# Performance work log

Measured on AMD Instinct MI355X. Metric: run time of the kernel, lower is better.

The kernel has to match this reference:

```python
import jax, jax.numpy as jnp
import numpy as np

NUM_BEAMS = 2


def setup_inputs() -> dict:
    key = jax.random.key(0)
    ks = jax.random.split(key, 5)
    B, T, H, E, F = 128, 32, 768, 4, 3072
    x = jax.random.normal(ks[0], (B, T, H), dtype=jnp.float32)
    Wg = jax.random.normal(ks[1], (E, H), dtype=jnp.float32) * (1.0 / np.sqrt(H))
    W1 = jax.random.normal(ks[2], (E, H, F), dtype=jnp.float32) * (1.0 / np.sqrt(H))
    b1 = jnp.zeros((E, F), dtype=jnp.float32)
    W2 = jax.random.normal(ks[3], (E, F, H), dtype=jnp.float32) * (1.0 / np.sqrt(F))
    b2 = jnp.zeros((E, H), dtype=jnp.float32)
    return {"x": x, "Wg": Wg, "W1": W1, "b1": b1, "W2": W2, "b2": b2}


def reference(x, Wg, W1, b1, W2, b2):
    B, T, H = x.shape
    E = Wg.shape[0]
    nb = NUM_BEAMS
    # ---- forward_gate: mask is all-ones, so masked mean == mean over tokens ----
    x_avg = jnp.mean(x, axis=1)                          # [B, H]
    logits_gate = x_avg @ Wg.T                           # [B, E]
    prob_gate = jax.nn.softmax(logits_gate, axis=-1)     # [B, E]
    # ---- importance auxiliary loss (torch.std uses ddof=1) ----
    importance = jnp.sum(prob_gate, axis=0)              # [E]
    importance_loss = (jnp.std(importance, ddof=1) / jnp.mean(importance)) ** 2
    # ---- beam search, first layer: exp(log(p)) == p, top-k per row ----
    current_scores = jnp.exp(jnp.log(prob_gate))         # == prob_gate (kept for fidelity)
    topk_values, gate_idx = jax.lax.top_k(current_scores, nb)   # [B, nb]
    beam_scores = topk_values.reshape(nb * B)            # row-major flatten, matches .view
    expert_route = gate_idx.reshape(nb * B)[:, None]     # [B*nb, 1]
    beam_idx = jnp.arange(nb * B)
    current_expert_select = expert_route[:, -1]          # [B*nb]
    # ---- first layer: replicate x and scores along beam dim (interleaved) ----
    x_rep = jnp.repeat(x, nb, axis=0)                    # [B*nb, T, H]
    scores_rep = jnp.repeat(prob_gate, nb, axis=0)       # [B*nb, E]
    # input_x = x_rep[beam_idx] is identity here (beam_idx == arange)
    # ---- forward_expert_ffn: run ALL experts, mask+combine with gate prob ----
    h1 = jnp.einsum('bth,ehf->betf', x_rep, W1) + b1[None, :, None, :]
    h1 = jax.nn.gelu(h1, approximate=False)              # torch GELU is exact erf form
    cand = jnp.einsum('betf,efh->beth', h1, W2) + b2[None, :, None, :]  # [B*nb, E, T, H]
    weight = scores_rep * jax.nn.one_hot(current_expert_select, E, dtype=scores_rep.dtype)
    output = jnp.einsum('beth,be->bth', cand, weight)    # weighted sum over experts
    return output, beam_scores, expert_route, beam_idx, importance_loss
```

## Files before the change

### kernel.cpp

```cpp
#include <hip/hip_runtime.h>
#include <math.h>

typedef _Float16 f16;
typedef _Float16 f16x8 __attribute__((ext_vector_type(8)));
typedef float f32x4 __attribute__((ext_vector_type(4)));

#define Bn 128
#define Tn 32
#define Hn 768
#define En 4
#define Fn 3072
#define Rn 256

static constexpr size_t OUT_ELEMS  = (size_t)Rn*Tn*Hn;
static constexpr size_t SCORES_OFF = OUT_ELEMS;
static constexpr size_t ROUTE_OFF  = OUT_ELEMS + Rn;
static constexpr size_t BIDX_OFF   = OUT_ELEMS + 2*Rn;
static constexpr size_t LOSS_OFF   = OUT_ELEMS + 3*Rn;

#define WS_WSF    0u
#define WS_ROUTE  4096u
#define WS_GRP    8192u
#define WS_X16    16384u
#define WS_W1T    (WS_X16 + 2u*Bn*Tn*Hn)
#define WS_W2T    (WS_W1T + 2u*En*Hn*Fn)
#define WS_H1     (WS_W2T + 2u*En*Fn*Hn)

#define GLOAD16(g, l) __builtin_amdgcn_global_load_lds( \
    (const __attribute__((address_space(1))) unsigned int*)(g), \
    (__attribute__((address_space(3))) unsigned int*)(l), 16, 0, 0)

__device__ __forceinline__ float fast_gelu(float v) {
  float s = v * 0.70710678118f;
  float a = fabsf(s);
  float t = 1.0f / (1.0f + 0.3275911f * a);
  float y = t*(0.254829592f + t*(-0.284496736f + t*(1.421413741f +
            t*(-1.453152027f + t*1.061405429f))));
  float er = 1.0f - y * __expf(-a*a);
  er = (s < 0.0f) ? -er : er;
  return 0.5f * v * (1.0f + er);
}

__global__ __launch_bounds__(64) void gate_kernel(
    const float* __restrict__ x, const float* __restrict__ Wg,
    float* __restrict__ out, float* __restrict__ wsf, int* __restrict__ route)
{
  const int b = blockIdx.x;
  const int l = threadIdx.x;
  float acc0=0.f, acc1=0.f, acc2=0.f, acc3=0.f;
  const float* xb = x + (size_t)b*Tn*Hn;
  for (int h = l; h < Hn; h += 64) {
    float xa = 0.f;
    #pragma unroll
    for (int t = 0; t < Tn; ++t) xa += xb[t*Hn + h];
    xa *= (1.0f/Tn);
    acc0 += xa * Wg[0*Hn + h];
    acc1 += xa * Wg[1*Hn + h];
    acc2 += xa * Wg[2*Hn + h];
    acc3 += xa * Wg[3*Hn + h];
  }
  #pragma unroll
  for (int o = 32; o > 0; o >>= 1) {
    acc0 += __shfl_down(acc0, o);
    acc1 += __shfl_down(acc1, o);
    acc2 += __shfl_down(acc2, o);
    acc3 += __shfl_down(acc3, o);
  }
  if (l == 0) {
    float lg[4] = {acc0, acc1, acc2, acc3};
    float m = fmaxf(fmaxf(lg[0],lg[1]), fmaxf(lg[2],lg[3]));
    float p[4]; float s = 0.f;
    #pragma unroll
    for (int e = 0; e < 4; ++e) { p[e] = expf(lg[e]-m); s += p[e]; }
    float inv = 1.f/s;
    #pragma unroll
    for (int e = 0; e < 4; ++e) { p[e] *= inv; wsf[b*4+e] = p[e]; }
    int i1 = 0;
    #pragma unroll
    for (int e = 1; e < 4; ++e) if (p[e] > p[i1]) i1 = e;
    int i2 = (i1 == 0) ? 1 : 0;
    #pragma unroll
    for (int e = 0; e < 4; ++e) if (e != i1 && p[e] > p[i2]) i2 = e;
    int idx[2] = {i1, i2};
    #pragma unroll
    for (int k = 0; k < 2; ++k) {
      int r = 2*b + k;
      float pv = p[idx[k]];
      wsf[512 + r] = pv;
      route[r] = idx[k];
      out[SCORES_OFF + r] = pv;
      out[ROUTE_OFF  + r] = (float)idx[k];
      out[BIDX_OFF   + r] = (float)r;
    }
  }
}

__global__ __launch_bounds__(64) void loss_kernel(
    const float* __restrict__ wsf, float* __restrict__ out)
{
  const int l = threadIdx.x;
  float i0=0.f,i1=0.f,i2=0.f,i3=0.f;
  for (int b = l; b < Bn; b += 64) {
    i0 += wsf[b*4+0]; i1 += wsf[b*4+1]; i2 += wsf[b*4+2]; i3 += wsf[b*4+3];
  }
  #pragma unroll
  for (int o = 32; o > 0; o >>= 1) {
    i0 += __shfl_down(i0,o); i1 += __shfl_down(i1,o);
    i2 += __shfl_down(i2,o); i3 += __shfl_down(i3,o);
  }
  if (l == 0) {
    float mean = 0.25f*(i0+i1+i2+i3);
    float d0=i0-mean, d1=i1-mean, d2=i2-mean, d3=i3-mean;
    float var = (d0*d0+d1*d1+d2*d2+d3*d3) * (1.f/3.f);
    out[LOSS_OFF] = var / (mean*mean);
  }
}

__global__ __launch_bounds__(64) void group_kernel(
    const int* __restrict__ route, int* __restrict__ grp)
{
  const int l = threadIdx.x;
  int cnt = 0;
  if (l < 4) { for (int r = 0; r < Rn; ++r) cnt += (route[r] == l); }
  int c0 = __shfl(cnt, 0), c1 = __shfl(cnt, 1), c2 = __shfl(cnt, 2), c3 = __shfl(cnt, 3);
  int off = (l >= 1 ? c0 : 0) + (l >= 2 ? c1 : 0) + (l >= 3 ? c2 : 0);
  if (l < 4) {
    int p = off;
    for (int r = 0; r < Rn; ++r) if (route[r] == l) grp[128 + p++] = r;
  }
  if (l == 0) {
    int cs[4] = {c0, c1, c2, c3};
    int os[4] = {0, c0, c0+c1, c0+c1+c2};
    int nt = 0;
    for (int e = 0; e < 4; ++e) {
      for (int s = 0; s < cs[e]; s += 8) {
        int nb = cs[e] - s; if (nb > 8) nb = 8;
        grp[8+nt*3+0] = e; grp[8+nt*3+1] = os[e]+s; grp[8+nt*3+2] = nb;
        ++nt;
      }
    }
    grp[0] = nt;
  }
}

__global__ __launch_bounds__(256) void convx_kernel(
    const float* __restrict__ x, f16* __restrict__ x16)
{
  const int i = (blockIdx.x*256 + threadIdx.x) * 8;
  float4 a = *(const float4*)(x + i);
  float4 b = *(const float4*)(x + i + 4);
  union { f16 h[8]; uint4 u; } p;
  p.h[0]=(f16)a.x; p.h[1]=(f16)a.y; p.h[2]=(f16)a.z; p.h[3]=(f16)a.w;
  p.h[4]=(f16)b.x; p.h[5]=(f16)b.y; p.h[6]=(f16)b.z; p.h[7]=(f16)b.w;
  *(uint4*)(x16 + i) = p.u;
}

__global__ __launch_bounds__(256) void transcvt_kernel(
    const float* __restrict__ src, f16* __restrict__ dst, int R, int C)
{
  __shared__ f16 t[64][74];
  const int e  = blockIdx.z;
  const int r0 = blockIdx.y*64, c0 = blockIdx.x*64;
  const float* s = src + (size_t)e*R*C;
  f16* d = dst + (size_t)e*R*C;
  const int tid = threadIdx.x;
  const int i  = tid >> 2;
  const int j0 = (tid & 3) * 16;
  #pragma unroll
  for (int q = 0; q < 16; q += 4) {
    float4 v = *(const float4*)(s + (size_t)(r0+i)*C + c0 + j0 + q);
    t[i][j0+q+0]=(f16)v.x; t[i][j0+q+1]=(f16)v.y; t[i][j0+q+2]=(f16)v.z; t[i][j0+q+3]=(f16)v.w;
  }
  __syncthreads();
  f16 o[16];
  #pragma unroll
  for (int q = 0; q < 16; ++q) o[q] = t[j0+q][i];
  *(uint4*)(d + (size_t)(c0+i)*R + r0 + j0)     = *(uint4*)&o[0];
  *(uint4*)(d + (size_t)(c0+i)*R + r0 + j0 + 8) = *(uint4*)&o[8];
}

template<int KD, int ND, int BN, int NI, bool G1>
__global__ __launch_bounds__(1024, 4) void gemm_kernel(
    const f16* __restrict__ A16, const f16* __restrict__ B16,
    const float* __restrict__ bias, f16* __restrict__ oh,
    float* __restrict__ of, const int* __restrict__ grp,
    const float* __restrict__ wsf)
{
  constexpr int NY = ND / BN;
  const int ntiles = grp[0];
  const int tix = blockIdx.x / NY;
  const int ny  = blockIdx.x % NY;
  if (tix >= ntiles) return;
  const int e      = grp[8+tix*3+0];
  const int bstart = grp[8+tix*3+1];
  const int nb     = grp[8+tix*3+2];
  const int n0     = ny * BN;
  const int tid    = threadIdx.x;
  const int lane   = tid & 63;
  const int w      = tid >> 6;

  extern __shared__ __align__(16) char smem[];
  constexpr int BNB = BN * 128;
  constexpr int BI  = BN / 128;
  constexpr int NLD = 2 + BI;

  const int srow8 = lane >> 3;
  const int sunit = (lane & 7) ^ srow8;
  const f16* asrc[2];
  #pragma unroll
  for (int i = 0; i < 2; ++i) {
    int row = (w*2 + i)*8 + srow8;
    int slot = row >> 5; if (slot >= nb) slot = nb - 1;
    int beam = grp[128 + bstart + slot];
    size_t rbase = G1 ? ((size_t)(beam>>1)*Tn + (row&31)) * (size_t)KD
                      : ((size_t)beam*Tn + (row&31)) * (size_t)KD;
    asrc[i] = A16 + rbase + sunit*8;
  }
  const f16* bsrc[BI];
  #pragma unroll
  for (int i = 0; i < BI; ++i) {
    int row = (w*BI + i)*8 + srow8;
    bsrc[i] = B16 + (size_t)e*ND*KD + (size_t)(n0 + row)*KD + sunit*8;
  }

  const int wm = w >> 2, wn = w & 3;
  const int lr = lane & 15, lk = lane >> 4;
  const int rowA0 = wm*64;
  const int rowB0 = wn*(NI*16);
  const int r7 = lr & 7;
  const int u0 = (lk ^ r7) * 16;

  constexpr int MI = 4;
  f32x4 acc[MI][NI];
  #pragma unroll
  for (int i=0;i<MI;++i)
    #pragma unroll
    for (int j=0;j<NI;++j) acc[i][j] = (f32x4){0.f,0.f,0.f,0.f};

  constexpr int NT = KD/64;

  auto STAGE = [&](int bsel, int kt2) {
    char* Ad = smem + bsel*32768 + (w*2)*1024;
    GLOAD16(asrc[0] + kt2*64, Ad);
    GLOAD16(asrc[1] + kt2*64, Ad + 1024);
    char* Bd = smem + 65536 + bsel*BNB + (w*BI)*1024;
    #pragma unroll
    for (int i = 0; i < BI; ++i) GLOAD16(bsrc[i] + kt2*64, Bd + i*1024);
  };

  STAGE(0, 0);

  int buf = 0;
  for (int kt = 0; kt < NT; ++kt) {
    if (kt + 1 < NT) {
      STAGE(buf ^ 1, kt + 1);
      asm volatile("s_waitcnt vmcnt(%0)" :: "i"(NLD) : "memory");
    } else {
      asm volatile("s_waitcnt vmcnt(0)" ::: "memory");
    }
    __builtin_amdgcn_sched_barrier(0);
    __builtin_amdgcn_s_barrier();
    __builtin_amdgcn_sched_barrier(0);

    const char* Ab = smem + buf*32768;
    const char* Bb = smem + 65536 + buf*BNB;
    #pragma unroll
    for (int ks = 0; ks < 2; ++ks) {
      const int ub = u0 ^ (ks << 6);
      f16x8 af[MI], bf[NI];
      #pragma unroll
      for (int mi=0;mi<MI;++mi)
        af[mi] = *(const f16x8*)(Ab + (rowA0 + mi*16 + lr)*128 + ub);
      #pragma unroll
      for (int ni=0;ni<NI;++ni)
        bf[ni] = *(const f16x8*)(Bb + (rowB0 + ni*16 + lr)*128 + ub);
      __builtin_amdgcn_s_setprio(1);
      #pragma unroll
      for (int mi=0;mi<MI;++mi)
        #pragma unroll
        for (int ni=0;ni<NI;++ni)
          acc[mi][ni] = __builtin_amdgcn_mfma_f32_16x16x32_f16(af[mi], bf[ni], acc[mi][ni], 0, 0, 0);
      __builtin_amdgcn_s_setprio(0);
    }
    __builtin_amdgcn_s_barrier();
    __builtin_amdgcn_sched_barrier(0);
    buf ^= 1;
  }

  const int nvalid = nb * Tn;
  char* cst = smem;

  if (G1) {
    float bvals[NI];
    #pragma unroll
    for (int ni=0;ni<NI;++ni) bvals[ni] = bias[e*ND + n0 + rowB0 + ni*16 + lr];
    #pragma unroll
    for (int mi=0;mi<MI;++mi){
      #pragma unroll
      for (int j=0;j<4;++j){
        const int m = rowA0 + mi*16 + (lane>>4)*4 + j;
        const int m7 = m & 7;
        #pragma unroll
        for (int ni=0;ni<NI;++ni){
          const int n = rowB0 + ni*16 + lr;
          float v = acc[mi][ni][j] + bvals[ni];
          f16 hv = (f16)fast_gelu(v);
          *(f16*)(cst + m*512 + (((n>>3)^m7)<<4) + (n&7)*2) = hv;
        }
      }
    }
  } else {
    #pragma unroll
    for (int mi=0;mi<MI;++mi){
      #pragma unroll
      for (int j=0;j<4;++j){
        const int m = rowA0 + mi*16 + (lane>>4)*4 + j;
        const int m7 = m & 7;
        #pragma unroll
        for (int ni=0;ni<NI;++ni){
          const int n = rowB0 + ni*16 + lr;
          *(float*)(cst + m*512 + (((n>>2)^m7)<<4) + (n&3)*4) = acc[mi][ni][j];
        }
      }
    }
  }
  __syncthreads();

  const int u  = tid & 31;
  const int tr = tid >> 5;
  if (G1) {
    #pragma unroll
    for (int it = 0; it < 8; ++it) {
      const int r = it*32 + tr;
      if (r >= nvalid) continue;
      const int beam = grp[128 + bstart + (r>>5)];
      uint4 v = *(const uint4*)(cst + r*512 + (((u&24)|((u&7)^(r&7)))<<4));
      *(uint4*)(oh + ((size_t)beam*Tn + (r&31))*(size_t)ND + n0 + u*8) = v;
    }
  } else {
    float4 b4 = *(const float4*)(bias + e*ND + n0 + u*4);
    #pragma unroll
    for (int it = 0; it < 8; ++it) {
      const int r = it*32 + tr;
      if (r >= nvalid) continue;
      const int beam = grp[128 + bstart + (r>>5)];
      const float sc = wsf[512 + beam];
      float4 v = *(const float4*)(cst + r*512 + (((u&24)|((u&7)^(r&7)))<<4));
      v.x = (v.x + b4.x)*sc; v.y = (v.y + b4.y)*sc;
      v.z = (v.z + b4.z)*sc; v.w = (v.w + b4.w)*sc;
      *(float4*)(of + ((size_t)beam*Tn + (r&31))*(size_t)Hn + n0 + u*4) = v;
    }
  }
}

extern "C" void kernel_launch(void* const* d_in, const int* in_sizes, int n_in,
                              void* d_out, int out_size, void* d_ws, size_t ws_size,
                              hipStream_t stream)
{
  const float* x  = (const float*)d_in[0];
  const float* Wg = (const float*)d_in[1];
  const float* W1 = (const float*)d_in[2];
  const float* b1 = (const float*)d_in[3];
  const float* W2 = (const float*)d_in[4];
  const float* b2 = (const float*)d_in[5];
  float* out = (float*)d_out;
  char* ws = (char*)d_ws;
  float* wsf  = (float*)(ws + WS_WSF);
  int*   route= (int*)(ws + WS_ROUTE);
  int*   grp  = (int*)(ws + WS_GRP);
  f16*   x16  = (f16*)(ws + WS_X16);
  f16*   w1t  = (f16*)(ws + WS_W1T);
  f16*   w2t  = (f16*)(ws + WS_W2T);
  f16*   h1   = (f16*)(ws + WS_H1);

  gate_kernel<<<Bn, 64, 0, stream>>>(x, Wg, out, wsf, route);
  group_kernel<<<1, 64, 0, stream>>>(route, grp);
  loss_kernel<<<1, 64, 0, stream>>>(wsf, out);
  convx_kernel<<<1536, 256, 0, stream>>>(x, x16);
  transcvt_kernel<<<dim3(48,12,4), 256, 0, stream>>>(W1, w1t, Hn, Fn);
  transcvt_kernel<<<dim3(12,48,4), 256, 0, stream>>>(W2, w2t, Fn, Hn);

  auto g1 = gemm_kernel<Hn, Fn, 256, 4, true>;
  auto g2 = gemm_kernel<Fn, Hn, 128, 2, false>;
  const int smB = 131072;
  hipFuncSetAttribute((const void*)g1, hipFuncAttributeMaxDynamicSharedMemorySize, smB);
  hipFuncSetAttribute((const void*)g2, hipFuncAttributeMaxDynamicSharedMemorySize, smB);
  g1<<<35*12, 1024, smB, stream>>>(x16, w1t, b1, h1, nullptr, grp, wsf);
  g2<<<35*6,  1024, smB, stream>>>(h1, w2t, b2, nullptr, out, grp, wsf);
}
```

Before: 200.0 us.

## Shrink GEMM tiles to 128 rows with fewer waves and smaller K step

Routing groups now hold 4 beams instead of 8, so each tile is 128 rows. Block size drops to 512 or 256 threads and the K step to 32, which cuts LDS to 48KB and 32KB. This should let several blocks share a CU and give more blocks for the small per-expert workloads. The epilogue is staged through LDS in two 64-row halves. Each tile now rereads the weights twice as often, and the shallow K step means more barriers per FLOP.

```diff
diff --git a/kernel.cpp b/kernel.cpp
--- a/kernel.cpp
+++ b/kernel.cpp
@@ -11,6 +11,7 @@
 #define En 4
 #define Fn 3072
 #define Rn 256
+#define MAXT 67
 
 static constexpr size_t OUT_ELEMS  = (size_t)Rn*Tn*Hn;
 static constexpr size_t SCORES_OFF = OUT_ELEMS;
@@ -126,15 +127,15 @@
   int off = (l >= 1 ? c0 : 0) + (l >= 2 ? c1 : 0) + (l >= 3 ? c2 : 0);
   if (l < 4) {
     int p = off;
-    for (int r = 0; r < Rn; ++r) if (route[r] == l) grp[128 + p++] = r;
+    for (int r = 0; r < Rn; ++r) if (route[r] == l) grp[384 + p++] = r;
   }
   if (l == 0) {
     int cs[4] = {c0, c1, c2, c3};
     int os[4] = {0, c0, c0+c1, c0+c1+c2};
     int nt = 0;
     for (int e = 0; e < 4; ++e) {
-      for (int s = 0; s < cs[e]; s += 8) {
-        int nb = cs[e] - s; if (nb > 8) nb = 8;
+      for (int s = 0; s < cs[e]; s += 4) {
+        int nb = cs[e] - s; if (nb > 4) nb = 4;
         grp[8+nt*3+0] = e; grp[8+nt*3+1] = os[e]+s; grp[8+nt*3+2] = nb;
         ++nt;
       }
@@ -179,14 +180,20 @@
   *(uint4*)(d + (size_t)(c0+i)*R + r0 + j0 + 8) = *(uint4*)&o[8];
 }
 
-template<int KD, int ND, int BN, int NI, bool G1>
-__global__ __launch_bounds__(1024, 4) void gemm_kernel(
+template<int KD, int ND, int BN, int NWAVE, bool G1>
+__global__ __launch_bounds__(NWAVE*64, 4) void gemm_kernel(
     const f16* __restrict__ A16, const f16* __restrict__ B16,
     const float* __restrict__ bias, f16* __restrict__ oh,
     float* __restrict__ of, const int* __restrict__ grp,
     const float* __restrict__ wsf)
 {
-  constexpr int NY = ND / BN;
+  constexpr int NY  = ND / BN;
+  constexpr int NWY = BN / 64;
+  constexpr int BI_A = 128 / (NWAVE*16);
+  constexpr int BI_B = BN  / (NWAVE*16);
+  constexpr int NLD  = BI_A + BI_B;
+  constexpr int BBUF = BN * 64;
+
   const int ntiles = grp[0];
   const int tix = blockIdx.x / NY;
   const int ny  = blockIdx.x % NY;
@@ -200,52 +207,47 @@
   const int w      = tid >> 6;
 
   extern __shared__ __align__(16) char smem[];
-  constexpr int BNB = BN * 128;
-  constexpr int BI  = BN / 128;
-  constexpr int NLD = 2 + BI;
-
-  const int srow8 = lane >> 3;
-  const int sunit = (lane & 7) ^ srow8;
-  const f16* asrc[2];
-  #pragma unroll
-  for (int i = 0; i < 2; ++i) {
-    int row = (w*2 + i)*8 + srow8;
+
+  const int srow  = lane >> 2;
+  const int sunit = (lane & 3) ^ ((lane >> 3) & 3);
+  const f16* asrc[BI_A];
+  #pragma unroll
+  for (int i = 0; i < BI_A; ++i) {
+    int row = (w*BI_A + i)*16 + srow;
     int slot = row >> 5; if (slot >= nb) slot = nb - 1;
-    int beam = grp[128 + bstart + slot];
+    int beam = grp[384 + bstart + slot];
     size_t rbase = G1 ? ((size_t)(beam>>1)*Tn + (row&31)) * (size_t)KD
                       : ((size_t)beam*Tn + (row&31)) * (size_t)KD;
     asrc[i] = A16 + rbase + sunit*8;
   }
-  const f16* bsrc[BI];
-  #pragma unroll
-  for (int i = 0; i < BI; ++i) {
-    int row = (w*BI + i)*8 + srow8;
+  const f16* bsrc[BI_B];
+  #pragma unroll
+  for (int i = 0; i < BI_B; ++i) {
+    int row = (w*BI_B + i)*16 + srow;
     bsrc[i] = B16 + (size_t)e*ND*KD + (size_t)(n0 + row)*KD + sunit*8;
   }
 
-  const int wm = w >> 2, wn = w & 3;
+  const int wm = w / NWY, wn = w % NWY;
   const int lr = lane & 15, lk = lane >> 4;
   const int rowA0 = wm*64;
-  const int rowB0 = wn*(NI*16);
-  const int r7 = lr & 7;
-  const int u0 = (lk ^ r7) * 16;
-
-  constexpr int MI = 4;
-  f32x4 acc[MI][NI];
-  #pragma unroll
-  for (int i=0;i<MI;++i)
-    #pragma unroll
-    for (int j=0;j<NI;++j) acc[i][j] = (f32x4){0.f,0.f,0.f,0.f};
-
-  constexpr int NT = KD/64;
+  const int rowB0 = wn*64;
+  const int ub = (lk ^ ((lr >> 1) & 3)) << 4;
+
+  f32x4 acc[4][4];
+  #pragma unroll
+  for (int i=0;i<4;++i)
+    #pragma unroll
+    for (int j=0;j<4;++j) acc[i][j] = (f32x4){0.f,0.f,0.f,0.f};
+
+  constexpr int NT = KD/32;
 
   auto STAGE = [&](int bsel, int kt2) {
-    char* Ad = smem + bsel*32768 + (w*2)*1024;
-    GLOAD16(asrc[0] + kt2*64, Ad);
-    GLOAD16(asrc[1] + kt2*64, Ad + 1024);
-    char* Bd = smem + 65536 + bsel*BNB + (w*BI)*1024;
-    #pragma unroll
-    for (int i = 0; i < BI; ++i) GLOAD16(bsrc[i] + kt2*64, Bd + i*1024);
+    char* Ad = smem + bsel*8192 + (w*BI_A)*1024;
+    #pragma unroll
+    for (int i = 0; i < BI_A; ++i) GLOAD16(asrc[i] + kt2*32, Ad + i*1024);
+    char* Bd = smem + 16384 + bsel*BBUF + (w*BI_B)*1024;
+    #pragma unroll
+    for (int i = 0; i < BI_B; ++i) GLOAD16(bsrc[i] + kt2*32, Bd + i*1024);
   };
 
   STAGE(0, 0);
@@ -262,26 +264,22 @@
     __builtin_amdgcn_s_barrier();
     __builtin_amdgcn_sched_barrier(0);
 
-    const char* Ab = smem + buf*32768;
-    const char* Bb = smem + 65536 + buf*BNB;
-    #pragma unroll
-    for (int ks = 0; ks < 2; ++ks) {
-      const int ub = u0 ^ (ks << 6);
-      f16x8 af[MI], bf[NI];
+    const char* Ab = smem + buf*8192;
+    const char* Bb = smem + 16384 + buf*BBUF;
+    f16x8 af[4], bf[4];
+    #pragma unroll
+    for (int mi=0;mi<4;++mi)
+      af[mi] = *(const f16x8*)(Ab + (rowA0 + mi*16 + lr)*64 + ub);
+    #pragma unroll
+    for (int ni=0;ni<4;++ni)
+      bf[ni] = *(const f16x8*)(Bb + (rowB0 + ni*16 + lr)*64 + ub);
+    __builtin_amdgcn_s_setprio(1);
+    #pragma unroll
+    for (int mi=0;mi<4;++mi)
       #pragma unroll
-      for (int mi=0;mi<MI;++mi)
-        af[mi] = *(const f16x8*)(Ab + (rowA0 + mi*16 + lr)*128 + ub);
-      #pragma unroll
-      for (int ni=0;ni<NI;++ni)
-        bf[ni] = *(const f16x8*)(Bb + (rowB0 + ni*16 + lr)*128 + ub);
-      __builtin_amdgcn_s_setprio(1);
-      #pragma unroll
-      for (int mi=0;mi<MI;++mi)
-        #pragma unroll
-        for (int ni=0;ni<NI;++ni)
-          acc[mi][ni] = __builtin_amdgcn_mfma_f32_16x16x32_f16(af[mi], bf[ni], acc[mi][ni], 0, 0, 0);
-      __builtin_amdgcn_s_setprio(0);
-    }
+      for (int ni=0;ni<4;++ni)
+        acc[mi][ni] = __builtin_amdgcn_mfma_f32_16x16x32_f16(af[mi], bf[ni], acc[mi][ni], 0, 0, 0);
+    __builtin_amdgcn_s_setprio(0);
     __builtin_amdgcn_s_barrier();
     __builtin_amdgcn_sched_barrier(0);
     buf ^= 1;
@@ -289,67 +287,58 @@
 
   const int nvalid = nb * Tn;
   char* cst = smem;
-
+  float bvals[4];
   if (G1) {
-    float bvals[NI];
-    #pragma unroll
-    for (int ni=0;ni<NI;++ni) bvals[ni] = bias[e*ND + n0 + rowB0 + ni*16 + lr];
-    #pragma unroll
-    for (int mi=0;mi<MI;++mi){
+    #pragma unroll
+    for (int ni=0;ni<4;++ni) bvals[ni] = bias[e*ND + n0 + rowB0 + ni*16 + lr];
+  }
+
+  #pragma unroll
+  for (int h = 0; h < 2; ++h) {
+    if (wm == h) {
       #pragma unroll
-      for (int j=0;j<4;++j){
-        const int m = rowA0 + mi*16 + (lane>>4)*4 + j;
-        const int m7 = m & 7;
+      for (int mi=0;mi<4;++mi){
         #pragma unroll
-        for (int ni=0;ni<NI;++ni){
-          const int n = rowB0 + ni*16 + lr;
-          float v = acc[mi][ni][j] + bvals[ni];
-          f16 hv = (f16)fast_gelu(v);
-          *(f16*)(cst + m*512 + (((n>>3)^m7)<<4) + (n&7)*2) = hv;
+        for (int j=0;j<4;++j){
+          const int m = mi*16 + (lane>>4)*4 + j;
+          const int m7 = m & 7;
+          #pragma unroll
+          for (int ni=0;ni<4;++ni){
+            const int n = rowB0 + ni*16 + lr;
+            if (G1) {
+              float v = acc[mi][ni][j] + bvals[ni];
+              *(f16*)(cst + m*512 + (((n>>3)^m7)<<4) + (n&7)*2) = (f16)fast_gelu(v);
+            } else {
+              *(float*)(cst + m*512 + (((n>>2)^m7)<<4) + (n&3)*4) = acc[mi][ni][j];
+            }
+          }
         }
       }
     }
-  } else {
-    #pragma unroll
-    for (int mi=0;mi<MI;++mi){
-      #pragma unroll
-      for (int j=0;j<4;++j){
-        const int m = rowA0 + mi*16 + (lane>>4)*4 + j;
-        const int m7 = m & 7;
-        #pragma unroll
-        for (int ni=0;ni<NI;++ni){
-          const int n = rowB0 + ni*16 + lr;
-          *(float*)(cst + m*512 + (((n>>2)^m7)<<4) + (n&3)*4) = acc[mi][ni][j];
+    __syncthreads();
+    const int u  = tid & 31;
+    const int tr = tid >> 5;
+    constexpr int RPI = NWAVE*2;
+    #pragma unroll
+    for (int it = 0; it < 64/RPI; ++it) {
+      const int rl = it*RPI + tr;
+      const int r  = h*64 + rl;
+      if (r < nvalid) {
+        const int beam = grp[384 + bstart + (r>>5)];
+        if (G1) {
+          uint4 v = *(const uint4*)(cst + rl*512 + (((u&24)|((u&7)^(rl&7)))<<4));
+          *(uint4*)(oh + ((size_t)beam*Tn + (r&31))*(size_t)ND + n0 + u*8) = v;
+        } else {
+          float4 b4 = *(const float4*)(bias + e*ND + n0 + u*4);
+          const float sc = wsf[512 + beam];
+          float4 v = *(const float4*)(cst + rl*512 + (((u&24)|((u&7)^(rl&7)))<<4));
+          v.x = (v.x + b4.x)*sc; v.y = (v.y + b4.y)*sc;
+          v.z = (v.z + b4.z)*sc; v.w = (v.w + b4.w)*sc;
+          *(float4*)(of + ((size_t)beam*Tn + (r&31))*(size_t)Hn + n0 + u*4) = v;
         }
       }
     }
-  }
-  __syncthreads();
-
-  const int u  = tid & 31;
-  const int tr = tid >> 5;
-  if (G1) {
-    #pragma unroll
-    for (int it = 0; it < 8; ++it) {
-      const int r = it*32 + tr;
-      if (r >= nvalid) continue;
-      const int beam = grp[128 + bstart + (r>>5)];
-      uint4 v = *(const uint4*)(cst + r*512 + (((u&24)|((u&7)^(r&7)))<<4));
-      *(uint4*)(oh + ((size_t)beam*Tn + (r&31))*(size_t)ND + n0 + u*8) = v;
-    }
-  } else {
-    float4 b4 = *(const float4*)(bias + e*ND + n0 + u*4);
-    #pragma unroll
-    for (int it = 0; it < 8; ++it) {
-      const int r = it*32 + tr;
-      if (r >= nvalid) continue;
-      const int beam = grp[128 + bstart + (r>>5)];
-      const float sc = wsf[512 + beam];
-      float4 v = *(const float4*)(cst + r*512 + (((u&24)|((u&7)^(r&7)))<<4));
-      v.x = (v.x + b4.x)*sc; v.y = (v.y + b4.y)*sc;
-      v.z = (v.z + b4.z)*sc; v.w = (v.w + b4.w)*sc;
-      *(float4*)(of + ((size_t)beam*Tn + (r&31))*(size_t)Hn + n0 + u*4) = v;
-    }
+    __syncthreads();
   }
 }
 
@@ -380,11 +369,12 @@
   transcvt_kernel<<<dim3(48,12,4), 256, 0, stream>>>(W1, w1t, Hn, Fn);
   transcvt_kernel<<<dim3(12,48,4), 256, 0, stream>>>(W2, w2t, Fn, Hn);
 
-  auto g1 = gemm_kernel<Hn, Fn, 256, 4, true>;
-  auto g2 = gemm_kernel<Fn, Hn, 128, 2, false>;
-  const int smB = 131072;
-  hipFuncSetAttribute((const void*)g1, hipFuncAttributeMaxDynamicSharedMemorySize, smB);
-  hipFuncSetAttribute((const void*)g2, hipFuncAttributeMaxDynamicSharedMemorySize, smB);
-  g1<<<35*12, 1024, smB, stream>>>(x16, w1t, b1, h1, nullptr, grp, wsf);
-  g2<<<35*6,  1024, smB, stream>>>(h1, w2t, b2, nullptr, out, grp, wsf);
-}
+  auto g1 = gemm_kernel<Hn, Fn, 256, 8, true>;
+  auto g2 = gemm_kernel<Fn, Hn, 128, 4, false>;
+  const int sm1 = 49152;
+  const int sm2 = 32768;
+  hipFuncSetAttribute((const void*)g1, hipFuncAttributeMaxDynamicSharedMemorySize, sm1);
+  hipFuncSetAttribute((const void*)g2, hipFuncAttributeMaxDynamicSharedMemorySize, sm2);
+  g1<<<MAXT*12, 512, sm1, stream>>>(x16, w1t, b1, h1, nullptr, grp, wsf);
+  g2<<<MAXT*6,  256, sm2, stream>>>(h1, w2t, b2, nullptr, out, grp, wsf);
+}
```

Result: slower. 213.4 us (+6.7%).
